# Performance work log

Hardware: AMD Instinct MI355X
Metric: run time of the kernel (lower is better)

Reference implementation:

```python
import jax, jax.numpy as jnp
import numpy as np

D = 256; NH = 8; NL = 4; NP = 4; DH = D // NH; DFFN = 1024; NQ = 900; BS = 4
SPATIAL = ((92, 92), (46, 46), (23, 23), (12, 12))  # (H, W) per level
LEVEL_START = (0, 8464, 10580, 11109)
S = sum(h * w for h, w in SPATIAL)  # 11253


def _ln(x, g, b):
    m = jnp.mean(x, -1, keepdims=True)
    v = jnp.var(x, -1, keepdims=True)
    return (x - m) / jnp.sqrt(v + 1e-5) * g + b


def setup_inputs() -> dict:
    key = jax.random.key(0)
    ks = jax.random.split(key, 24)
    p = lambda k, s: 0.02 * jax.random.normal(k, s, jnp.float32)
    return {
        "tgt": jax.random.normal(ks[0], (NQ, BS, D), jnp.float32),
        "tgt_query_pos": jax.random.normal(ks[1], (NQ, BS, D), jnp.float32),
        "tgt_reference_points": jax.random.uniform(ks[2], (NQ, BS, NL, 2), jnp.float32),
        "memory": jax.random.normal(ks[3], (S, BS, D), jnp.float32),
        "memory_spatial_shapes": jnp.array(SPATIAL, jnp.int32),
        "memory_level_start_index": jnp.array(LEVEL_START, jnp.int32),
        "in_proj_w": p(ks[4], (3 * D, D)), "in_proj_b": p(ks[5], (3 * D,)),
        "out_proj_w": p(ks[6], (D, D)), "out_proj_b": p(ks[7], (D,)),
        "off_w": p(ks[8], (NH * NL * NP * 2, D)), "off_b": p(ks[9], (NH * NL * NP * 2,)),
        "aw_w": p(ks[10], (NH * NL * NP, D)), "aw_b": p(ks[11], (NH * NL * NP,)),
        "vproj_w": p(ks[12], (D, D)), "vproj_b": p(ks[13], (D,)),
        "oproj_w": p(ks[14], (D, D)), "oproj_b": p(ks[15], (D,)),
        "ln1_g": jnp.ones((D,), jnp.float32), "ln1_b": jnp.zeros((D,), jnp.float32),
        "ln2_g": jnp.ones((D,), jnp.float32), "ln2_b": jnp.zeros((D,), jnp.float32),
        "ln3_g": jnp.ones((D,), jnp.float32), "ln3_b": jnp.zeros((D,), jnp.float32),
        "lin1_w": p(ks[16], (DFFN, D)), "lin1_b": p(ks[17], (DFFN,)),
        "lin2_w": p(ks[18], (D, DFFN)), "lin2_b": p(ks[19], (D,)),
    }


def _self_attn(q, k, v, in_w, in_b, out_w, out_b):
    # q, k, v: (nq, bs, d) -- torch nn.MultiheadAttention, eval mode
    wq, wk, wv = jnp.split(in_w, 3, axis=0)
    bq, bk, bv = jnp.split(in_b, 3)
    qp = (q @ wq.T + bq).reshape(NQ, BS, NH, DH)
    kp = (k @ wk.T + bk).reshape(NQ, BS, NH, DH)
    vp = (v @ wv.T + bv).reshape(NQ, BS, NH, DH)
    s = jnp.einsum("qbhd,kbhd->bhqk", qp, kp) / jnp.sqrt(jnp.float32(DH))
    a = jax.nn.softmax(s, axis=-1)
    o = jnp.einsum("bhqk,kbhd->qbhd", a, vp).reshape(NQ, BS, D)
    return o @ out_w.T + out_b


def _msdeform(x, ref, mem, off_w, off_b, aw_w, aw_b, vproj_w, vproj_b, oproj_w, oproj_b):
    # x: (bs, nq, d); ref: (bs, nq, nl, 2) in [0,1]; mem: (bs, S, d)
    value = (mem @ vproj_w.T + vproj_b).reshape(BS, S, NH, DH)
    off = (x @ off_w.T + off_b).reshape(BS, NQ, NH, NL, NP, 2)
    aw = jax.nn.softmax((x @ aw_w.T + aw_b).reshape(BS, NQ, NH, NL * NP), axis=-1)
    aw = aw.reshape(BS, NQ, NH, NL, NP)
    # offset normalizer = (W, H) per level
    norm = jnp.array([[w, h] for (h, w) in SPATIAL], jnp.float32)
    loc = ref[:, :, None, :, None, :] + off / norm[None, None, None, :, None, :]
    out = jnp.zeros((BS, NH, NQ, DH), x.dtype)
    for l, (H, W) in enumerate(SPATIAL):
        s0 = LEVEL_START[l]
        v = value[:, s0:s0 + H * W].transpose(0, 2, 1, 3)  # (bs, nh, H*W, dh)
        g = loc[:, :, :, l].transpose(0, 2, 1, 3, 4)       # (bs, nh, nq, np, 2)
        # grid_sample align_corners=False, padding_mode='zeros'
        px = g[..., 0] * W - 0.5
        py = g[..., 1] * H - 0.5
        x0 = jnp.floor(px).astype(jnp.int32)
        y0 = jnp.floor(py).astype(jnp.int32)
        wx = px - x0
        wy = py - y0
        samp = jnp.zeros((BS, NH, NQ, NP, DH), x.dtype)
        for dx, dy, w in ((0, 0, (1 - wx) * (1 - wy)), (1, 0, wx * (1 - wy)),
                          (0, 1, (1 - wx) * wy), (1, 1, wx * wy)):
            xi = x0 + dx
            yi = y0 + dy
            valid = ((xi >= 0) & (xi < W) & (yi >= 0) & (yi < H)).astype(x.dtype)
            idx = (jnp.clip(yi, 0, H - 1) * W + jnp.clip(xi, 0, W - 1)).reshape(BS, NH, NQ * NP)
            gat = jnp.take_along_axis(v, idx[..., None], axis=2).reshape(BS, NH, NQ, NP, DH)
            samp = samp + (w * valid)[..., None] * gat
        a = aw[:, :, :, l].transpose(0, 2, 1, 3)  # (bs, nh, nq, np)
        out = out + (samp * a[..., None]).sum(axis=3)
    out = out.transpose(0, 2, 1, 3).reshape(BS, NQ, D)
    return out @ oproj_w.T + oproj_b


def reference(tgt, tgt_query_pos, tgt_reference_points, memory,
              memory_spatial_shapes, memory_level_start_index,
              in_proj_w, in_proj_b, out_proj_w, out_proj_b,
              off_w, off_b, aw_w, aw_b, vproj_w, vproj_b, oproj_w, oproj_b,
              ln1_g, ln1_b, ln2_g, ln2_b, ln3_g, ln3_b,
              lin1_w, lin1_b, lin2_w, lin2_b):
    # module_seq = ['sa', 'ca', 'ffn']; dropout inactive (eval)
    q = tgt + tgt_query_pos
    tgt2 = _self_attn(q, q, tgt, in_proj_w, in_proj_b, out_proj_w, out_proj_b)
    tgt = _ln(tgt + tgt2, ln2_g, ln2_b)
    x = (tgt + tgt_query_pos).transpose(1, 0, 2)
    ref = tgt_reference_points.transpose(1, 0, 2, 3)
    mem = memory.transpose(1, 0, 2)
    tgt2 = _msdeform(x, ref, mem, off_w, off_b, aw_w, aw_b,
                     vproj_w, vproj_b, oproj_w, oproj_b).transpose(1, 0, 2)
    tgt = _ln(tgt + tgt2, ln1_g, ln1_b)
    ff = jax.nn.relu(tgt @ lin1_w.T + lin1_b) @ lin2_w.T + lin2_b
    return _ln(tgt + ff, ln3_g, ln3_b)
```

## Files before the change

### kernel.cpp

```cpp
#include <hip/hip_runtime.h>
#include <math.h>

#define D_MODEL 256
#define NHEAD   8
#define NLVL    4
#define NPTS    4
#define DHEAD   32
#define DFFN    1024
#define NQ      900
#define BSZ     4
#define NROW    (NQ * BSZ)
#define NROWP   3648
#define S_TOT   11253
#define VROWS   (S_TOT * BSZ)
#define SASCALE 0.17677669529663687f

typedef __attribute__((ext_vector_type(8))) short short8;
typedef __attribute__((ext_vector_type(4))) float f32x4;
typedef unsigned short ushort_t;

static __device__ __forceinline__ unsigned f2bf1(float f) {
    unsigned u = __float_as_uint(f);
    return (u + 0x7FFFu + ((u >> 16) & 1u)) >> 16;
}
static __device__ __forceinline__ unsigned pack2bf(float x, float y) {
    return f2bf1(x) | (f2bf1(y) << 16);
}
static __device__ __forceinline__ float bf2f(ushort_t u) {
    return __uint_as_float(((unsigned)u) << 16);
}

#if __has_builtin(__builtin_amdgcn_global_load_lds)
#define HAS_GLL 1
#endif

static __device__ __forceinline__ void stage_w16(const ushort_t* g, ushort_t* ldsbase, int lane)
{
#ifdef HAS_GLL
    __builtin_amdgcn_global_load_lds(
        (const __attribute__((address_space(1))) unsigned int*)g,
        (__attribute__((address_space(3))) unsigned int*)ldsbase, 16, 0, 0);
#else
    *(uint4*)(ldsbase + lane * 8) = *(const uint4*)g;
#endif
}

#define WAIT_VM_BAR(N) do {                                            \
    asm volatile("s_waitcnt vmcnt(" #N ") lgkmcnt(0)" ::: "memory");   \
    __builtin_amdgcn_sched_barrier(0);                                 \
    __builtin_amdgcn_s_barrier(); } while (0)

#define LK_BAR() do {                                                  \
    asm volatile("s_waitcnt lgkmcnt(0)" ::: "memory");                 \
    __builtin_amdgcn_sched_barrier(0);                                 \
    __builtin_amdgcn_s_barrier(); } while (0)

#define WB_IN   0
#define WB_VP   196608
#define WB_OUTP 262144
#define WB_OFF  327680
#define WB_AW   393216
#define WB_OP   425984
#define WB_L1   491520
#define WB_L2   753664
#define WB_TOT  1015808

__global__ __launch_bounds__(256) void cvt_weights(
    const float* __restrict__ w_in, const float* __restrict__ w_vp,
    const float* __restrict__ w_outp, const float* __restrict__ w_off,
    const float* __restrict__ w_aw, const float* __restrict__ w_op,
    const float* __restrict__ w_l1, const float* __restrict__ w_l2,
    ushort_t* __restrict__ dst,
    const float* __restrict__ tgt, const float* __restrict__ qpos,
    ushort_t* __restrict__ tgt16, ushort_t* __restrict__ tq16)
{
    int b = blockIdx.x;
    if (b < 496) {
        const float* src;
        int dstoff;
        int kbits = 8;
        if (b < 96)       { src = w_in;   dstoff = WB_IN;   }
        else if (b < 128) { src = w_vp;   b -= 96;  dstoff = WB_VP;   }
        else if (b < 160) { src = w_outp; b -= 128; dstoff = WB_OUTP; }
        else if (b < 192) { src = w_off;  b -= 160; dstoff = WB_OFF;  }
        else if (b < 208) { src = w_aw;   b -= 192; dstoff = WB_AW;   }
        else if (b < 240) { src = w_op;   b -= 208; dstoff = WB_OP;   }
        else if (b < 368) { src = w_l1;   b -= 240; dstoff = WB_L1;   }
        else              { src = w_l2;   b -= 368; dstoff = WB_L2;   kbits = 10; }
        int i = (b * 256 + threadIdx.x) * 8;
        float4 f0 = *(const float4*)(src + i);
        float4 f1 = *(const float4*)(src + i + 4);
        uint4 u;
        u.x = pack2bf(f0.x, f0.y); u.y = pack2bf(f0.z, f0.w);
        u.z = pack2bf(f1.x, f1.y); u.w = pack2bf(f1.z, f1.w);
        int K = 1 << kbits;
        int n = i >> kbits;
        int k = i & (K - 1);
        int kswz = (k & ~63) | ((k & 63) ^ ((n & 7) << 3));
        *(uint4*)(dst + dstoff + (size_t)n * K + kswz) = u;
    } else {
        int bb = b - 496;
        ushort_t* dbuf = tgt16;
        bool addq = false;
        if (bb >= 456) { bb -= 456; dbuf = tq16; addq = true; }
        int i = bb * 2048 + threadIdx.x * 8;
        int row = i >> 8, k = i & 255;
        uint4 u = make_uint4(0u, 0u, 0u, 0u);
        if (row < NROW) {
            const float* sp = tgt + (size_t)row * 256 + k;
            float4 f0 = *(const float4*)(sp + 0);
            float4 f1 = *(const float4*)(sp + 4);
            if (addq) {
                const float* qp = qpos + (size_t)row * 256 + k;
                float4 q0 = *(const float4*)(qp + 0);
                float4 q1 = *(const float4*)(qp + 4);
                f0.x += q0.x; f0.y += q0.y; f0.z += q0.z; f0.w += q0.w;
                f1.x += q1.x; f1.y += q1.y; f1.z += q1.z; f1.w += q1.w;
            }
            u.x = pack2bf(f0.x, f0.y); u.y = pack2bf(f0.z, f0.w);
            u.z = pack2bf(f1.x, f1.y); u.w = pack2bf(f1.z, f1.w);
        }
        int kswz = (k & ~63) | ((k & 63) ^ ((row & 7) << 3));
        *(uint4*)(dbuf + (size_t)row * 256 + kswz) = u;
    }
}

__global__ __launch_bounds__(256) void proj_fused(
    const ushort_t* __restrict__ tq16, const ushort_t* __restrict__ tgt16,
    const ushort_t* __restrict__ in_wb, const float* __restrict__ in_b,
    const float* __restrict__ mem, const ushort_t* __restrict__ vp_wb,
    const float* __restrict__ vp_b,
    ushort_t* __restrict__ qkv16, ushort_t* __restrict__ value16)
{
    __shared__ ushort_t As[2][64 * 64];
    __shared__ ushort_t Ws[2][256 * 64];

    const int t    = threadIdx.x;
    const int bid  = blockIdx.x;
    const int wv   = t >> 6;
    const int ln   = t & 63;
    const int L    = ln & 15;
    const int quad = ln >> 4;
    const int swz  = (L & 7) << 3;
    const int lrow = ln >> 3;
    const int lchk = (ln & 7) << 3;

    if (bid < 684) {
        const int m0 = (bid % 57) * 64;
        const int n0 = (bid / 57) * 64;
        const float oscale = (n0 < 256) ? SASCALE : 1.f;
        const ushort_t* Ab = (n0 < 512) ? tq16 : tgt16;

        auto stageQ = [&](int k0, int buf) {
#pragma unroll
            for (int j = 0; j < 2; ++j) {
                int r0 = (wv * 2 + j) * 8;
                stage_w16(Ab + (size_t)(m0 + r0 + lrow) * 256 + k0 + lchk, &As[buf][r0 * 64], ln);
                stage_w16(in_wb + (size_t)(n0 + r0 + lrow) * 256 + k0 + lchk, &Ws[buf][r0 * 64], ln);
            }
        };

        f32x4 acc[4] = {{0.f,0.f,0.f,0.f},{0.f,0.f,0.f,0.f},
                        {0.f,0.f,0.f,0.f},{0.f,0.f,0.f,0.f}};

        stageQ(0, 0);
        int cur = 0;
        for (int k = 0; k < 4; ++k) {
            if (k < 3) { stageQ((k + 1) * 64, cur ^ 1); WAIT_VM_BAR(4); }
            else       { WAIT_VM_BAR(0); }
#pragma unroll
            for (int kh = 0; kh < 2; ++kh) {
                int ko = (kh * 32 + quad * 8) ^ swz;
                short8 af = *(const short8*)&As[cur][(wv * 16 + L) * 64 + ko];
#pragma unroll
                for (int cb = 0; cb < 4; ++cb) {
                    short8 bf = *(const short8*)&Ws[cur][(cb * 16 + L) * 64 + ko];
                    acc[cb] = __builtin_amdgcn_mfma_f32_16x16x32_bf16(af, bf, acc[cb], 0, 0, 0);
                }
            }
            __builtin_amdgcn_s_barrier();
            cur ^= 1;
        }
#pragma unroll
        for (int cb = 0; cb < 4; ++cb) {
            int col = n0 + cb * 16 + L;
            float bv = in_b[col];
#pragma unroll
            for (int i = 0; i < 4; ++i) {
                int m = m0 + wv * 16 + quad * 4 + i;
                if (m < NROW)
                    qkv16[(size_t)m * 768 + col] = (ushort_t)f2bf1((acc[cb][i] + bv) * oscale);
            }
        }
    } else {
        const int vb = bid - 684;
        const int m0 = vb * 64;
        const int trow = t >> 2;
        const int tk   = (t & 3) << 4;
        const int wsz  = (trow & 7) << 3;

        const int  mrow = m0 + trow;
        const bool mv   = (mrow < VROWS);
        const float* arow = mem + (size_t)mrow * 256 + tk;

        auto stageWv = [&](int k0, int buf) {
#pragma unroll
            for (int j = 0; j < 8; ++j) {
                int r0 = (wv * 8 + j) * 8;
                stage_w16(vp_wb + (size_t)(r0 + lrow) * 256 + k0 + lchk, &Ws[buf][r0 * 64], ln);
            }
        };
        auto stageAv = [&](int k0, int buf) {
            uint4 u0, u1;
            if (mv) {
                const float* ap = arow + k0;
                float4 a0 = *(const float4*)(ap + 0);
                float4 a1 = *(const float4*)(ap + 4);
                float4 a2 = *(const float4*)(ap + 8);
                float4 a3 = *(const float4*)(ap + 12);
                u0.x = pack2bf(a0.x, a0.y); u0.y = pack2bf(a0.z, a0.w);
                u0.z = pack2bf(a1.x, a1.y); u0.w = pack2bf(a1.z, a1.w);
                u1.x = pack2bf(a2.x, a2.y); u1.y = pack2bf(a2.z, a2.w);
                u1.z = pack2bf(a3.x, a3.y); u1.w = pack2bf(a3.z, a3.w);
            } else {
                u0 = make_uint4(0u, 0u, 0u, 0u); u1 = u0;
            }
            *(uint4*)&As[buf][trow * 64 + (tk ^ wsz)]       = u0;
            *(uint4*)&As[buf][trow * 64 + ((tk + 8) ^ wsz)] = u1;
        };

        f32x4 acc[16];
#pragma unroll
        for (int i = 0; i < 16; ++i) acc[i] = (f32x4){0.f, 0.f, 0.f, 0.f};

        stageWv(0, 0);
        stageAv(0, 0);
        int cur = 0;
        for (int k = 0; k < 4; ++k) {
            if (k < 3) { stageWv((k + 1) * 64, cur ^ 1); WAIT_VM_BAR(8); }
            else       { WAIT_VM_BAR(0); }
#pragma unroll
            for (int kh = 0; kh < 2; ++kh) {
                int ko = (kh * 32 + quad * 8) ^ swz;
                short8 af = *(const short8*)&As[cur][(wv * 16 + L) * 64 + ko];
#pragma unroll
                for (int cb = 0; cb < 16; ++cb) {
                    short8 bf = *(const short8*)&Ws[cur][(cb * 16 + L) * 64 + ko];
                    acc[cb] = __builtin_amdgcn_mfma_f32_16x16x32_bf16(af, bf, acc[cb], 0, 0, 0);
                }
            }
            if (k < 3) stageAv((k + 1) * 64, cur ^ 1);
            __builtin_amdgcn_s_barrier();
            cur ^= 1;
        }

        ushort_t* Cs = Ws[0];
#pragma unroll
        for (int half = 0; half < 2; ++half) {
            if (half) __syncthreads();
#pragma unroll
            for (int cb = 0; cb < 8; ++cb) {
                int col = cb * 16 + L;
                float bv = vp_b[half * 128 + col];
#pragma unroll
                for (int i = 0; i < 4; ++i) {
                    int r = wv * 16 + quad * 4 + i;
                    Cs[r * 136 + col] = (ushort_t)f2bf1(acc[half * 8 + cb][i] + bv);
                }
            }
            __syncthreads();
            {
                int r  = t >> 2;
                int ch = (t & 3) * 32;
                int m  = m0 + r;
                if (m < VROWS) {
                    const ushort_t* src = &Cs[r * 136 + ch];
                    uint4* dst = (uint4*)(value16 + (size_t)m * 256 + half * 128 + ch);
#pragma unroll
                    for (int j = 0; j < 4; ++j)
                        dst[j] = *(const uint4*)(src + j * 8);
                }
            }
        }
    }
}

__global__ __launch_bounds__(256) void sa_flash16(
    const ushort_t* __restrict__ qkv, ushort_t* __restrict__ attn_out)
{
    __shared__ ushort_t Ks[2 * 2080];
    __shared__ ushort_t Vt[2 * 2304];
    __shared__ ushort_t Ps[4 * 1152];

    const int t    = threadIdx.x;
    const int q0   = blockIdx.x * 64;
    const int b    = blockIdx.y & 3;
    const int h    = blockIdx.y >> 2;
    const int wv   = t >> 6;
    const int ln   = t & 63;
    const int L    = ln & 15;
    const int quad = ln >> 4;

    union { uint4 u; short8 s; } qu;
    qu.u = make_uint4(0u, 0u, 0u, 0u);
    {
        int q = q0 + wv * 16 + L;
        if (q < NQ)
            qu.u = *(const uint4*)(qkv + ((size_t)q * 4 + b) * 768 + h * 32 + quad * 8);
    }
    const short8 qf = qu.s;

    float mrun = -1e30f, lrun = 0.f;
    f32x4 oacc[2] = {{0.f,0.f,0.f,0.f},{0.f,0.f,0.f,0.f}};

    const int skey = t >> 2;
    const int sdg  = t & 3;

    uint4 ku, vu;
    auto kv_load = [&](int k0) {
        int kg = k0 + skey;
        ku = make_uint4(0u, 0u, 0u, 0u);
        vu = make_uint4(0u, 0u, 0u, 0u);
        if (kg < NQ) {
            const ushort_t* base = qkv + ((size_t)kg * 4 + b) * 768 + 256 + h * 32 + sdg * 8;
            ku = *(const uint4*)base;
            vu = *(const uint4*)(base + 256);
        }
    };

    kv_load(0);
    int it = 0;
    for (int k0 = 0; k0 < NQ; k0 += 64, it ^= 1) {
        *(uint4*)&Ks[it * 2080 + sdg * 520 + skey * 8] = ku;
        {
            ushort_t* vp = &Vt[it * 2304 + sdg * 8 * 72 + skey];
            vp[0 * 72] = (ushort_t)(vu.x & 0xffffu);
            vp[1 * 72] = (ushort_t)(vu.x >> 16);
            vp[2 * 72] = (ushort_t)(vu.y & 0xffffu);
            vp[3 * 72] = (ushort_t)(vu.y >> 16);
            vp[4 * 72] = (ushort_t)(vu.z & 0xffffu);
            vp[5 * 72] = (ushort_t)(vu.z >> 16);
            vp[6 * 72] = (ushort_t)(vu.w & 0xffffu);
            vp[7 * 72] = (ushort_t)(vu.w >> 16);
        }
        __syncthreads();
        if (k0 + 64 < NQ) kv_load(k0 + 64);

        f32x4 sacc[4] = {{0.f,0.f,0.f,0.f},{0.f,0.f,0.f,0.f},
                         {0.f,0.f,0.f,0.f},{0.f,0.f,0.f,0.f}};
#pragma unroll
        for (int cb = 0; cb < 4; ++cb) {
            short8 kf = *(const short8*)&Ks[it * 2080 + quad * 520 + (cb * 16 + L) * 8];
            sacc[cb] = __builtin_amdgcn_mfma_f32_16x16x32_bf16(kf, qf, sacc[cb], 0, 0, 0);
        }
        if (k0 + 64 > NQ) {
#pragma unroll
            for (int cb = 0; cb < 4; ++cb)
#pragma unroll
                for (int i = 0; i < 4; ++i)
                    if (k0 + cb * 16 + quad * 4 + i >= NQ) sacc[cb][i] = -1e30f;
        }

        float ml = -1e30f;
#pragma unroll
        for (int cb = 0; cb < 4; ++cb)
#pragma unroll
            for (int i = 0; i < 4; ++i) ml = fmaxf(ml, sacc[cb][i]);
        ml = fmaxf(ml, __shfl_xor(ml, 16, 64));
        ml = fmaxf(ml, __shfl_xor(ml, 32, 64));
        float mnew  = fmaxf(mrun, ml);
        float alpha = __expf(mrun - mnew);
        float p[16];
        float rs = 0.f;
#pragma unroll
        for (int cb = 0; cb < 4; ++cb)
#pragma unroll
            for (int i = 0; i < 4; ++i) {
                float e = __expf(sacc[cb][i] - mnew);
                p[cb * 4 + i] = e;
                rs += e;
            }
        rs += __shfl_xor(rs, 16, 64);
        rs += __shfl_xor(rs, 32, 64);
        lrun = lrun * alpha + rs;
        mrun = mnew;

        {
            ushort_t* pw = &Ps[wv * 1152 + L * 72];
#pragma unroll
            for (int cb = 0; cb < 4; ++cb) {
                uint2 u;
                u.x = pack2bf(p[cb * 4 + 0], p[cb * 4 + 1]);
                u.y = pack2bf(p[cb * 4 + 2], p[cb * 4 + 3]);
                *(uint2*)&pw[cb * 16 + quad * 4] = u;
            }
        }
#pragma unroll
        for (int i = 0; i < 4; ++i) {
            float ai = __shfl(alpha, quad * 4 + i, 64);
            oacc[0][i] *= ai;
            oacc[1][i] *= ai;
        }
        __syncthreads();

#pragma unroll
        for (int ks = 0; ks < 2; ++ks) {
            short8 pf = *(const short8*)&Ps[wv * 1152 + L * 72 + ks * 32 + quad * 8];
#pragma unroll
            for (int db = 0; db < 2; ++db) {
                short8 vf = *(const short8*)&Vt[it * 2304 + (db * 16 + L) * 72 + ks * 32 + quad * 8];
                oacc[db] = __builtin_amdgcn_mfma_f32_16x16x32_bf16(pf, vf, oacc[db], 0, 0, 0);
            }
        }
    }

#pragma unroll
    for (int i = 0; i < 4; ++i) {
        float lq = __shfl(lrun, quad * 4 + i, 64);
        float li = 1.f / lq;
        int q = q0 + wv * 16 + quad * 4 + i;
        if (q < NQ) {
            ushort_t* op = attn_out + ((size_t)q * 4 + b) * 256 + h * 32 + L;
            op[0]  = (ushort_t)f2bf1(oacc[0][i] * li);
            op[16] = (ushort_t)f2bf1(oacc[1][i] * li);
        }
    }
}

__global__ __launch_bounds__(512, 1) void fused_ca(
    const ushort_t* __restrict__ att16,
    const float* __restrict__ tgt, const float* __restrict__ qpos,
    const ushort_t* __restrict__ outp_wb, const float* __restrict__ outp_b,
    const float* __restrict__ ln2g, const float* __restrict__ ln2b,
    const ushort_t* __restrict__ off_wb, const float* __restrict__ off_b,
    const ushort_t* __restrict__ aw_wb, const float* __restrict__ aw_b,
    const float* __restrict__ refp,
    float* __restrict__ tgt_a, float* __restrict__ px_g,
    float* __restrict__ py_g, float* __restrict__ aw_g)
{
    __shared__ ushort_t Ws[2][256 * 64];
    __shared__ ushort_t att_s[16 * 264];
    __shared__ ushort_t xca_s[16 * 264];
    __shared__ float    aws_s[16 * 128];
    __shared__ float    sS[8][16], s2S[8][16];

    const int t    = threadIdx.x;
    const int m0   = blockIdx.x * 16;
    const int wv   = t >> 6;
    const int ln   = t & 63;
    const int L    = ln & 15;
    const int quad = ln >> 4;
    const int swz  = (L & 7) << 3;
    const int lrow = ln >> 3;
    const int lchk = (ln & 7) << 3;
    const int rloc = quad * 4;

    auto stage4 = [&](const ushort_t* base, int buf) {
#pragma unroll
        for (int j = 0; j < 4; ++j) {
            int r0 = (wv * 4 + j) * 8;
            stage_w16(base + (size_t)(r0 + lrow) * 256 + lchk, &Ws[buf][r0 * 64], ln);
        }
    };
    auto stage2 = [&](const ushort_t* base, int buf) {
#pragma unroll
        for (int j = 0; j < 2; ++j) {
            int r0 = (wv * 2 + j) * 8;
            stage_w16(base + (size_t)(r0 + lrow) * 256 + lchk, &Ws[buf][r0 * 64], ln);
        }
    };
    auto mfma2 = [&](const ushort_t* A, int koff, int buf, f32x4* acc) {
#pragma unroll
        for (int kh = 0; kh < 2; ++kh) {
            int ko = (kh * 32 + quad * 8) ^ swz;
            short8 af = *(const short8*)&A[L * 264 + koff + kh * 32 + quad * 8];
#pragma unroll
            for (int cb = 0; cb < 2; ++cb) {
                short8 bf = *(const short8*)&Ws[buf][(wv * 32 + cb * 16 + L) * 64 + ko];
                acc[cb] = __builtin_amdgcn_mfma_f32_16x16x32_bf16(af, bf, acc[cb], 0, 0, 0);
            }
        }
    };

    {
        int r = t >> 5, s = (t & 31) * 8;
        *(uint4*)&att_s[r * 264 + s] = *(const uint4*)(att16 + (size_t)(m0 + r) * 256 + s);
    }
    stage4(outp_wb, 0);
    int cur = 0;

    {
        f32x4 acc[2] = {{0.f,0.f,0.f,0.f},{0.f,0.f,0.f,0.f}};
        for (int k = 0; k < 4; ++k) {
            if (k < 3) stage4(outp_wb + (k + 1) * 64, cur ^ 1);
            else       stage4(off_wb, cur ^ 1);
            WAIT_VM_BAR(4);
            mfma2(att_s, k * 64, cur, acc);
            __builtin_amdgcn_s_barrier();
            cur ^= 1;
        }
        float s[4] = {0.f,0.f,0.f,0.f}, s2v[4] = {0.f,0.f,0.f,0.f};
#pragma unroll
        for (int cb = 0; cb < 2; ++cb) {
            int col = wv * 32 + cb * 16 + L;
            float bv = outp_b[col];
#pragma unroll
            for (int i = 0; i < 4; ++i) {
                float xv = acc[cb][i] + bv + tgt[(size_t)(m0 + rloc + i) * 256 + col];
                acc[cb][i] = xv;
                s[i] += xv; s2v[i] += xv * xv;
            }
        }
#pragma unroll
        for (int off = 1; off < 16; off <<= 1)
#pragma unroll
            for (int i = 0; i < 4; ++i) {
                s[i]   += __shfl_xor(s[i],   off, 64);
                s2v[i] += __shfl_xor(s2v[i], off, 64);
            }
        if (L == 0)
#pragma unroll
            for (int i = 0; i < 4; ++i) { sS[wv][rloc + i] = s[i]; s2S[wv][rloc + i] = s2v[i]; }
        LK_BAR();
        float mean[4], rstd[4];
#pragma unroll
        for (int i = 0; i < 4; ++i) {
            float St = 0.f, S2t = 0.f;
#pragma unroll
            for (int w = 0; w < 8; ++w) { St += sS[w][rloc + i]; S2t += s2S[w][rloc + i]; }
            mean[i] = St * (1.f / 256.f);
            float var = S2t * (1.f / 256.f) - mean[i] * mean[i];
            rstd[i] = rsqrtf(var + 1e-5f);
        }
#pragma unroll
        for (int cb = 0; cb < 2; ++cb) {
            int col = wv * 32 + cb * 16 + L;
            float gv = ln2g[col], bt = ln2b[col];
#pragma unroll
            for (int i = 0; i < 4; ++i) {
                float y = (acc[cb][i] - mean[i]) * rstd[i] * gv + bt;
                tgt_a[(size_t)(m0 + rloc + i) * 256 + col] = y;
                xca_s[(rloc + i) * 264 + col] =
                    (ushort_t)f2bf1(y + qpos[(size_t)(m0 + rloc + i) * 256 + col]);
            }
        }
    }

    {
        f32x4 acc[2] = {{0.f,0.f,0.f,0.f},{0.f,0.f,0.f,0.f}};
        for (int k = 0; k < 4; ++k) {
            if (k < 3) { stage4(off_wb + (k + 1) * 64, cur ^ 1); WAIT_VM_BAR(4); }
            else       { stage2(aw_wb, cur ^ 1);                 WAIT_VM_BAR(2); }
            mfma2(xca_s, k * 64, cur, acc);
            __builtin_amdgcn_s_barrier();
            cur ^= 1;
        }
        const float dims[4] = {92.f, 46.f, 23.f, 12.f};
#pragma unroll
        for (int cb = 0; cb < 2; ++cb) {
            int col = wv * 32 + cb * 16 + L;
            float bv = off_b[col];
            int hh = col >> 5, lp = (col & 31) >> 1, isY = col & 1;
            int l = lp >> 2;
            float dim = dims[l];
            float* dst = isY ? py_g : px_g;
#pragma unroll
            for (int i = 0; i < 4; ++i) {
                int row = m0 + rloc + i;
                float ref = refp[((size_t)row * 4 + l) * 2 + isY];
                dst[(size_t)row * 128 + hh * 16 + lp] = ref * dim + (acc[cb][i] + bv) - 0.5f;
            }
        }
    }

    {
        f32x4 acc = {0.f, 0.f, 0.f, 0.f};
        for (int k = 0; k < 4; ++k) {
            if (k < 3) { stage2(aw_wb + (k + 1) * 64, cur ^ 1); WAIT_VM_BAR(2); }
            else       { WAIT_VM_BAR(0); }
#pragma unroll
            for (int kh = 0; kh < 2; ++kh) {
                int ko = (kh * 32 + quad * 8) ^ swz;
                short8 af = *(const short8*)&xca_s[L * 264 + k * 64 + kh * 32 + quad * 8];
                short8 bf = *(const short8*)&Ws[cur][(wv * 16 + L) * 64 + ko];
                acc = __builtin_amdgcn_mfma_f32_16x16x32_bf16(af, bf, acc, 0, 0, 0);
            }
            __builtin_amdgcn_s_barrier();
            cur ^= 1;
        }
        {
            int col = wv * 16 + L;
            float bv = aw_b[col];
#pragma unroll
            for (int i = 0; i < 4; ++i)
                aws_s[(rloc + i) * 128 + col] = acc[i] + bv;
        }
        LK_BAR();
    }

    if (t < 128) {
        int r = t >> 3, hh = t & 7;
        float v[16];
        float m = -1e30f;
#pragma unroll
        for (int j = 0; j < 16; ++j) { v[j] = aws_s[r * 128 + hh * 16 + j]; m = fmaxf(m, v[j]); }
        float ssum = 0.f;
#pragma unroll
        for (int j = 0; j < 16; ++j) { v[j] = __expf(v[j] - m); ssum += v[j]; }
        float inv = 1.f / ssum;
#pragma unroll
        for (int j = 0; j < 16; ++j)
            aw_g[(size_t)(m0 + r) * 128 + hh * 16 + j] = v[j] * inv;
    }
}

__global__ __launch_bounds__(256) void msdeform4(
    const float* __restrict__ px_g, const float* __restrict__ py_g,
    const float* __restrict__ aw_g, const ushort_t* __restrict__ value16,
    ushort_t* __restrict__ out)
{
    const int t   = threadIdx.x;
    const int row = blockIdx.x * 4 + (t >> 6);
    const int ln  = t & 63;
    const int h   = ln >> 3;
    const int d   = (ln & 7) * 4;
    const int b   = row & 3;

    const int HsI[4] = {92, 46, 23, 12};
    const int S0_[4] = {0, 8464, 10580, 11109};

    const ushort_t* vb = value16 + (size_t)b * 256 + h * 32 + d;
    const float* pxr = px_g + (size_t)row * 128 + h * 16;
    const float* pyr = py_g + (size_t)row * 128 + h * 16;
    const float* awr = aw_g + (size_t)row * 128 + h * 16;

    float a0 = 0.f, a1 = 0.f, a2 = 0.f, a3 = 0.f;
#pragma unroll
    for (int l = 0; l < 4; ++l) {
        const int H = HsI[l], W = HsI[l], base = S0_[l];
#pragma unroll
        for (int p = 0; p < 4; ++p) {
            const int lp = l * 4 + p;
            float px = pxr[lp], py = pyr[lp], aw = awr[lp];
            float x0f = floorf(px), y0f = floorf(py);
            int x0 = (int)x0f, y0 = (int)y0f;
            float wx = px - x0f, wy = py - y0f;
            float s0 = 0.f, s1 = 0.f, s2 = 0.f, s3 = 0.f;
#pragma unroll
            for (int dy = 0; dy < 2; ++dy) {
#pragma unroll
                for (int dx = 0; dx < 2; ++dx) {
                    int xi = x0 + dx, yi = y0 + dy;
                    float flag = (xi >= 0 && xi < W && yi >= 0 && yi < H) ? 1.f : 0.f;
                    int xc = xi < 0 ? 0 : (xi >= W ? W - 1 : xi);
                    int yc = yi < 0 ? 0 : (yi >= H ? H - 1 : yi);
                    float wgt = (dx ? wx : 1.f - wx) * (dy ? wy : 1.f - wy) * flag;
                    uint2 gv = *(const uint2*)(vb + (size_t)(base + yc * W + xc) * 1024);
                    s0 = fmaf(wgt, bf2f((ushort_t)(gv.x & 0xffffu)), s0);
                    s1 = fmaf(wgt, bf2f((ushort_t)(gv.x >> 16)), s1);
                    s2 = fmaf(wgt, bf2f((ushort_t)(gv.y & 0xffffu)), s2);
                    s3 = fmaf(wgt, bf2f((ushort_t)(gv.y >> 16)), s3);
                }
            }
            a0 = fmaf(aw, s0, a0);
            a1 = fmaf(aw, s1, a1);
            a2 = fmaf(aw, s2, a2);
            a3 = fmaf(aw, s3, a3);
        }
    }
    uint2 u;
    u.x = pack2bf(a0, a1);
    u.y = pack2bf(a2, a3);
    *(uint2*)(out + (size_t)row * 256 + h * 32 + d) = u;
}

__global__ __launch_bounds__(512, 1) void ffn_fused(
    const ushort_t* __restrict__ att2_16,
    const float* __restrict__ tgt_a,
    const ushort_t* __restrict__ op_wb, const float* __restrict__ op_b,
    const float* __restrict__ ln1g, const float* __restrict__ ln1b,
    const ushort_t* __restrict__ l1_wb, const float* __restrict__ l1b,
    const ushort_t* __restrict__ l2_wb, const float* __restrict__ l2b,
    const float* __restrict__ ln3g, const float* __restrict__ ln3b,
    float* __restrict__ out)
{
    __shared__ ushort_t Ws[2][256 * 64];
    __shared__ ushort_t A1[16 * 264];
    __shared__ ushort_t hc[16 * 264];
    __shared__ float    sS[8][16], s2S[8][16];

    const int t    = threadIdx.x;
    const int m0   = blockIdx.x * 16;
    const int wv   = t >> 6;
    const int ln   = t & 63;
    const int L    = ln & 15;
    const int quad = ln >> 4;
    const int swz  = (L & 7) << 3;
    const int lrow = ln >> 3;
    const int lchk = (ln & 7) << 3;
    const int rloc = quad * 4;

    auto stageWs = [&](const ushort_t* base, int stride, int buf) {
#pragma unroll
        for (int j = 0; j < 4; ++j) {
            int r0 = (wv * 4 + j) * 8;
            stage_w16(base + (size_t)(r0 + lrow) * stride + lchk, &Ws[buf][r0 * 64], ln);
        }
    };
    auto mfma2 = [&](const ushort_t* A, int koff, int buf, f32x4* acc) {
#pragma unroll
        for (int kh = 0; kh < 2; ++kh) {
            int ko = (kh * 32 + quad * 8) ^ swz;
            short8 af = *(const short8*)&A[L * 264 + koff + kh * 32 + quad * 8];
#pragma unroll
            for (int cb = 0; cb < 2; ++cb) {
                short8 bf = *(const short8*)&Ws[buf][(wv * 32 + cb * 16 + L) * 64 + ko];
                acc[cb] = __builtin_amdgcn_mfma_f32_16x16x32_bf16(af, bf, acc[cb], 0, 0, 0);
            }
        }
    };

    {
        int r = t >> 5, s = (t & 31) * 8;
        *(uint4*)&hc[r * 264 + s] = *(const uint4*)(att2_16 + (size_t)(m0 + r) * 256 + s);
    }
    stageWs(op_wb, 256, 0);
    int cur = 0;

    f32x4 resid[2];

    {
        f32x4 acc[2] = {{0.f,0.f,0.f,0.f},{0.f,0.f,0.f,0.f}};
        for (int k = 0; k < 4; ++k) {
            if (k < 3) stageWs(op_wb + (k + 1) * 64, 256, cur ^ 1);
            else       stageWs(l1_wb, 256, cur ^ 1);
            WAIT_VM_BAR(4);
            mfma2(hc, k * 64, cur, acc);
            __builtin_amdgcn_s_barrier();
            cur ^= 1;
        }
        float s[4] = {0.f,0.f,0.f,0.f}, s2v[4] = {0.f,0.f,0.f,0.f};
#pragma unroll
        for (int cb = 0; cb < 2; ++cb) {
            int col = wv * 32 + cb * 16 + L;
            float bv = op_b[col];
#pragma unroll
            for (int i = 0; i < 4; ++i) {
                float xv = acc[cb][i] + bv + tgt_a[(size_t)(m0 + rloc + i) * 256 + col];
                acc[cb][i] = xv;
                s[i] += xv; s2v[i] += xv * xv;
            }
        }
#pragma unroll
        for (int off = 1; off < 16; off <<= 1)
#pragma unroll
            for (int i = 0; i < 4; ++i) {
                s[i]   += __shfl_xor(s[i],   off, 64);
                s2v[i] += __shfl_xor(s2v[i], off, 64);
            }
        if (L == 0)
#pragma unroll
            for (int i = 0; i < 4; ++i) { sS[wv][rloc + i] = s[i]; s2S[wv][rloc + i] = s2v[i]; }
        LK_BAR();
        float mean[4], rstd[4];
#pragma unroll
        for (int i = 0; i < 4; ++i) {
            float St = 0.f, S2t = 0.f;
#pragma unroll
            for (int w = 0; w < 8; ++w) { St += sS[w][rloc + i]; S2t += s2S[w][rloc + i]; }
            mean[i] = St * (1.f / 256.f);
            float var = S2t * (1.f / 256.f) - mean[i] * mean[i];
            rstd[i] = rsqrtf(var + 1e-5f);
        }
#pragma unroll
        for (int cb = 0; cb < 2; ++cb) {
            int col = wv * 32 + cb * 16 + L;
            float gv = ln1g[col], bt = ln1b[col];
#pragma unroll
            for (int i = 0; i < 4; ++i) {
                float y = (acc[cb][i] - mean[i]) * rstd[i] * gv + bt;
                resid[cb][i] = y;
                A1[(rloc + i) * 264 + col] = (ushort_t)f2bf1(y);
            }
        }
    }

    f32x4 accf[2] = {{0.f,0.f,0.f,0.f},{0.f,0.f,0.f,0.f}};
    for (int c = 0; c < 4; ++c) {
        f32x4 acch[2] = {{0.f,0.f,0.f,0.f},{0.f,0.f,0.f,0.f}};
        for (int k = 0; k < 4; ++k) {
            if (k < 3) stageWs(l1_wb + (size_t)(c * 256) * 256 + (k + 1) * 64, 256, cur ^ 1);
            else       stageWs(l2_wb + c * 256, 1024, cur ^ 1);
            WAIT_VM_BAR(4);
            mfma2(A1, k * 64, cur, acch);
            __builtin_amdgcn_s_barrier();
            cur ^= 1;
        }
#pragma unroll
        for (int cb = 0; cb < 2; ++cb) {
            int colc = wv * 32 + cb * 16 + L;
            float bv = l1b[c * 256 + colc];
#pragma unroll
            for (int i = 0; i < 4; ++i)
                hc[(rloc + i) * 264 + colc] = (ushort_t)f2bf1(fmaxf(acch[cb][i] + bv, 0.f));
        }
        LK_BAR();
        for (int k = 0; k < 4; ++k) {
            if (k < 3)      { stageWs(l2_wb + c * 256 + (k + 1) * 64, 1024, cur ^ 1); WAIT_VM_BAR(4); }
            else if (c < 3) { stageWs(l1_wb + (size_t)((c + 1) * 256) * 256, 256, cur ^ 1); WAIT_VM_BAR(4); }
            else            { WAIT_VM_BAR(0); }
            mfma2(hc, k * 64, cur, accf);
            __builtin_amdgcn_s_barrier();
            cur ^= 1;
        }
    }

    {
        float s[4] = {0.f,0.f,0.f,0.f}, s2v[4] = {0.f,0.f,0.f,0.f};
#pragma unroll
        for (int cb = 0; cb < 2; ++cb) {
            int col = wv * 32 + cb * 16 + L;
            float bv = l2b[col];
#pragma unroll
            for (int i = 0; i < 4; ++i) {
                float xv = accf[cb][i] + bv + resid[cb][i];
                accf[cb][i] = xv;
                s[i] += xv; s2v[i] += xv * xv;
            }
        }
#pragma unroll
        for (int off = 1; off < 16; off <<= 1)
#pragma unroll
            for (int i = 0; i < 4; ++i) {
                s[i]   += __shfl_xor(s[i],   off, 64);
                s2v[i] += __shfl_xor(s2v[i], off, 64);
            }
        if (L == 0)
#pragma unroll
            for (int i = 0; i < 4; ++i) { sS[wv][rloc + i] = s[i]; s2S[wv][rloc + i] = s2v[i]; }
        LK_BAR();
        float mean[4], rstd[4];
#pragma unroll
        for (int i = 0; i < 4; ++i) {
            float St = 0.f, S2t = 0.f;
#pragma unroll
            for (int w = 0; w < 8; ++w) { St += sS[w][rloc + i]; S2t += s2S[w][rloc + i]; }
            mean[i] = St * (1.f / 256.f);
            float var = S2t * (1.f / 256.f) - mean[i] * mean[i];
            rstd[i] = rsqrtf(var + 1e-5f);
        }
#pragma unroll
        for (int cb = 0; cb < 2; ++cb) {
            int col = wv * 32 + cb * 16 + L;
            float gv = ln3g[col], bt = ln3b[col];
#pragma unroll
            for (int i = 0; i < 4; ++i) {
                float y = (accf[cb][i] - mean[i]) * rstd[i] * gv + bt;
                out[(size_t)(m0 + rloc + i) * 256 + col] = y;
            }
        }
    }
}

extern "C" void kernel_launch(void* const* d_in, const int* in_sizes, int n_in,
                              void* d_out, int out_size, void* d_ws, size_t ws_size,
                              hipStream_t stream)
{
    const float* tgt    = (const float*)d_in[0];
    const float* qpos   = (const float*)d_in[1];
    const float* refp   = (const float*)d_in[2];
    const float* mem    = (const float*)d_in[3];
    const float* in_w   = (const float*)d_in[6];
    const float* in_b   = (const float*)d_in[7];
    const float* outp_w = (const float*)d_in[8];
    const float* outp_b = (const float*)d_in[9];
    const float* off_w  = (const float*)d_in[10];
    const float* off_b  = (const float*)d_in[11];
    const float* aw_w   = (const float*)d_in[12];
    const float* aw_b   = (const float*)d_in[13];
    const float* vp_w   = (const float*)d_in[14];
    const float* vp_b   = (const float*)d_in[15];
    const float* op_w   = (const float*)d_in[16];
    const float* op_b   = (const float*)d_in[17];
    const float* ln1g   = (const float*)d_in[18];
    const float* ln1b   = (const float*)d_in[19];
    const float* ln2g   = (const float*)d_in[20];
    const float* ln2b   = (const float*)d_in[21];
    const float* ln3g   = (const float*)d_in[22];
    const float* ln3b   = (const float*)d_in[23];
    const float* l1w    = (const float*)d_in[24];
    const float* l1b    = (const float*)d_in[25];
    const float* l2w    = (const float*)d_in[26];
    const float* l2b    = (const float*)d_in[27];
    float* out = (float*)d_out;
    float* ws  = (float*)d_ws;

    ushort_t* qkv16    = (ushort_t*)ws;
    ushort_t* att16    = (ushort_t*)(ws + 691200);
    float*    tgt_a    = ws + 1843200;
    ushort_t* tgt16    = (ushort_t*)(ws + 1843200);
    ushort_t* tq16     = (ushort_t*)(ws + 2310144);
    float*    px_g     = ws + 2995200;
    float*    py_g     = ws + 3456000;
    float*    aw_g     = ws + 3916800;
    ushort_t* att2_16  = (ushort_t*)(ws + 4377600);
    ushort_t* value16  = (ushort_t*)(ws + 5760000);
    ushort_t* wb       = (ushort_t*)(ws + 13364736);

    const ushort_t* in_wb   = wb + WB_IN;
    const ushort_t* vp_wb   = wb + WB_VP;
    const ushort_t* outp_wb = wb + WB_OUTP;
    const ushort_t* off_wb  = wb + WB_OFF;
    const ushort_t* aw_wb   = wb + WB_AW;
    const ushort_t* op_wb   = wb + WB_OP;
    const ushort_t* l1_wb   = wb + WB_L1;
    const ushort_t* l2_wb   = wb + WB_L2;

    dim3 b256(256);

    hipLaunchKernelGGL(cvt_weights, dim3(1408), b256, 0, stream,
                       in_w, vp_w, outp_w, off_w, aw_w, op_w, l1w, l2w, wb,
                       tgt, qpos, tgt16, tq16);
    hipLaunchKernelGGL(proj_fused, dim3(1388), b256, 0, stream,
                       tq16, tgt16, in_wb, in_b, mem, vp_wb, vp_b, qkv16, value16);
    hipLaunchKernelGGL(sa_flash16, dim3(15, 32), b256, 0, stream, qkv16, att16);
    hipLaunchKernelGGL(fused_ca, dim3(225), dim3(512), 0, stream,
                       att16, tgt, qpos, outp_wb, outp_b, ln2g, ln2b,
                       off_wb, off_b, aw_wb, aw_b, refp,
                       tgt_a, px_g, py_g, aw_g);
    hipLaunchKernelGGL(msdeform4, dim3(900), b256, 0, stream,
                       px_g, py_g, aw_g, value16, att2_16);
    hipLaunchKernelGGL(ffn_fused, dim3(225), dim3(512), 0, stream,
                       att2_16, tgt_a, op_wb, op_b, ln1g, ln1b,
                       l1_wb, l1b, l2_wb, l2b, ln3g, ln3b, out);
}
```

Measured before the change: 242.9 us.

## Split projection kernel, halve weight LDS tiles, add MFMA priority hints

Splits the fused QKV/value projection kernel into two separate kernels so the QKV blocks no longer reserve the large 256-row weight LDS buffer. The fused_ca and ffn_fused kernels stage weights in 128-row halves instead of 256-row tiles, which halves their weight LDS footprint but doubles the number of staging/barrier steps. s_setprio hints are added around the MFMA sections in the flash attention kernel. The aim is higher occupancy from a smaller LDS footprint, at the cost of an extra launch and more synchronization rounds.

```diff
diff --git a/kernel.cpp b/kernel.cpp
--- a/kernel.cpp
+++ b/kernel.cpp
@@ -125,18 +125,15 @@
     }
 }
 
-__global__ __launch_bounds__(256) void proj_fused(
+__global__ __launch_bounds__(256) void proj_qkv(
     const ushort_t* __restrict__ tq16, const ushort_t* __restrict__ tgt16,
     const ushort_t* __restrict__ in_wb, const float* __restrict__ in_b,
-    const float* __restrict__ mem, const ushort_t* __restrict__ vp_wb,
-    const float* __restrict__ vp_b,
-    ushort_t* __restrict__ qkv16, ushort_t* __restrict__ value16)
+    ushort_t* __restrict__ qkv16)
 {
     __shared__ ushort_t As[2][64 * 64];
-    __shared__ ushort_t Ws[2][256 * 64];
+    __shared__ ushort_t Ws[2][64 * 64];
 
     const int t    = threadIdx.x;
-    const int bid  = blockIdx.x;
     const int wv   = t >> 6;
     const int ln   = t & 63;
     const int L    = ln & 15;
@@ -145,141 +142,155 @@
     const int lrow = ln >> 3;
     const int lchk = (ln & 7) << 3;
 
-    if (bid < 684) {
-        const int m0 = (bid % 57) * 64;
-        const int n0 = (bid / 57) * 64;
-        const float oscale = (n0 < 256) ? SASCALE : 1.f;
-        const ushort_t* Ab = (n0 < 512) ? tq16 : tgt16;
-
-        auto stageQ = [&](int k0, int buf) {
-#pragma unroll
-            for (int j = 0; j < 2; ++j) {
-                int r0 = (wv * 2 + j) * 8;
-                stage_w16(Ab + (size_t)(m0 + r0 + lrow) * 256 + k0 + lchk, &As[buf][r0 * 64], ln);
-                stage_w16(in_wb + (size_t)(n0 + r0 + lrow) * 256 + k0 + lchk, &Ws[buf][r0 * 64], ln);
-            }
-        };
-
-        f32x4 acc[4] = {{0.f,0.f,0.f,0.f},{0.f,0.f,0.f,0.f},
-                        {0.f,0.f,0.f,0.f},{0.f,0.f,0.f,0.f}};
-
-        stageQ(0, 0);
-        int cur = 0;
-        for (int k = 0; k < 4; ++k) {
-            if (k < 3) { stageQ((k + 1) * 64, cur ^ 1); WAIT_VM_BAR(4); }
-            else       { WAIT_VM_BAR(0); }
-#pragma unroll
-            for (int kh = 0; kh < 2; ++kh) {
-                int ko = (kh * 32 + quad * 8) ^ swz;
-                short8 af = *(const short8*)&As[cur][(wv * 16 + L) * 64 + ko];
-#pragma unroll
-                for (int cb = 0; cb < 4; ++cb) {
-                    short8 bf = *(const short8*)&Ws[cur][(cb * 16 + L) * 64 + ko];
-                    acc[cb] = __builtin_amdgcn_mfma_f32_16x16x32_bf16(af, bf, acc[cb], 0, 0, 0);
-                }
-            }
-            __builtin_amdgcn_s_barrier();
-            cur ^= 1;
-        }
-#pragma unroll
-        for (int cb = 0; cb < 4; ++cb) {
-            int col = n0 + cb * 16 + L;
-            float bv = in_b[col];
-#pragma unroll
-            for (int i = 0; i < 4; ++i) {
-                int m = m0 + wv * 16 + quad * 4 + i;
-                if (m < NROW)
-                    qkv16[(size_t)m * 768 + col] = (ushort_t)f2bf1((acc[cb][i] + bv) * oscale);
-            }
-        }
-    } else {
-        const int vb = bid - 684;
-        const int m0 = vb * 64;
-        const int trow = t >> 2;
-        const int tk   = (t & 3) << 4;
-        const int wsz  = (trow & 7) << 3;
-
-        const int  mrow = m0 + trow;
-        const bool mv   = (mrow < VROWS);
-        const float* arow = mem + (size_t)mrow * 256 + tk;
-
-        auto stageWv = [&](int k0, int buf) {
-#pragma unroll
-            for (int j = 0; j < 8; ++j) {
-                int r0 = (wv * 8 + j) * 8;
-                stage_w16(vp_wb + (size_t)(r0 + lrow) * 256 + k0 + lchk, &Ws[buf][r0 * 64], ln);
-            }
-        };
-        auto stageAv = [&](int k0, int buf) {
-            uint4 u0, u1;
-            if (mv) {
-                const float* ap = arow + k0;
-                float4 a0 = *(const float4*)(ap + 0);
-                float4 a1 = *(const float4*)(ap + 4);
-                float4 a2 = *(const float4*)(ap + 8);
-                float4 a3 = *(const float4*)(ap + 12);
-                u0.x = pack2bf(a0.x, a0.y); u0.y = pack2bf(a0.z, a0.w);
-                u0.z = pack2bf(a1.x, a1.y); u0.w = pack2bf(a1.z, a1.w);
-                u1.x = pack2bf(a2.x, a2.y); u1.y = pack2bf(a2.z, a2.w);
-                u1.z = pack2bf(a3.x, a3.y); u1.w = pack2bf(a3.z, a3.w);
-            } else {
-                u0 = make_uint4(0u, 0u, 0u, 0u); u1 = u0;
-            }
-            *(uint4*)&As[buf][trow * 64 + (tk ^ wsz)]       = u0;
-            *(uint4*)&As[buf][trow * 64 + ((tk + 8) ^ wsz)] = u1;
-        };
-
-        f32x4 acc[16];
-#pragma unroll
-        for (int i = 0; i < 16; ++i) acc[i] = (f32x4){0.f, 0.f, 0.f, 0.f};
-
-        stageWv(0, 0);
-        stageAv(0, 0);
-        int cur = 0;
-        for (int k = 0; k < 4; ++k) {
-            if (k < 3) { stageWv((k + 1) * 64, cur ^ 1); WAIT_VM_BAR(8); }
-            else       { WAIT_VM_BAR(0); }
-#pragma unroll
-            for (int kh = 0; kh < 2; ++kh) {
-                int ko = (kh * 32 + quad * 8) ^ swz;
-                short8 af = *(const short8*)&As[cur][(wv * 16 + L) * 64 + ko];
-#pragma unroll
-                for (int cb = 0; cb < 16; ++cb) {
-                    short8 bf = *(const short8*)&Ws[cur][(cb * 16 + L) * 64 + ko];
-                    acc[cb] = __builtin_amdgcn_mfma_f32_16x16x32_bf16(af, bf, acc[cb], 0, 0, 0);
-                }
-            }
-            if (k < 3) stageAv((k + 1) * 64, cur ^ 1);
-            __builtin_amdgcn_s_barrier();
-            cur ^= 1;
-        }
-
-        ushort_t* Cs = Ws[0];
-#pragma unroll
-        for (int half = 0; half < 2; ++half) {
-            if (half) __syncthreads();
-#pragma unroll
-            for (int cb = 0; cb < 8; ++cb) {
-                int col = cb * 16 + L;
-                float bv = vp_b[half * 128 + col];
-#pragma unroll
-                for (int i = 0; i < 4; ++i) {
-                    int r = wv * 16 + quad * 4 + i;
-                    Cs[r * 136 + col] = (ushort_t)f2bf1(acc[half * 8 + cb][i] + bv);
-                }
-            }
-            __syncthreads();
-            {
-                int r  = t >> 2;
-                int ch = (t & 3) * 32;
-                int m  = m0 + r;
-                if (m < VROWS) {
-                    const ushort_t* src = &Cs[r * 136 + ch];
-                    uint4* dst = (uint4*)(value16 + (size_t)m * 256 + half * 128 + ch);
-#pragma unroll
-                    for (int j = 0; j < 4; ++j)
-                        dst[j] = *(const uint4*)(src + j * 8);
-                }
+    const int m0 = (blockIdx.x % 57) * 64;
+    const int n0 = (blockIdx.x / 57) * 64;
+    const float oscale = (n0 < 256) ? SASCALE : 1.f;
+    const ushort_t* Ab = (n0 < 512) ? tq16 : tgt16;
+
+    auto stageQ = [&](int k0, int buf) {
+#pragma unroll
+        for (int j = 0; j < 2; ++j) {
+            int r0 = (wv * 2 + j) * 8;
+            stage_w16(Ab + (size_t)(m0 + r0 + lrow) * 256 + k0 + lchk, &As[buf][r0 * 64], ln);
+            stage_w16(in_wb + (size_t)(n0 + r0 + lrow) * 256 + k0 + lchk, &Ws[buf][r0 * 64], ln);
+        }
+    };
+
+    f32x4 acc[4] = {{0.f,0.f,0.f,0.f},{0.f,0.f,0.f,0.f},
+                    {0.f,0.f,0.f,0.f},{0.f,0.f,0.f,0.f}};
+
+    stageQ(0, 0);
+    int cur = 0;
+    for (int k = 0; k < 4; ++k) {
+        if (k < 3) { stageQ((k + 1) * 64, cur ^ 1); WAIT_VM_BAR(4); }
+        else       { WAIT_VM_BAR(0); }
+#pragma unroll
+        for (int kh = 0; kh < 2; ++kh) {
+            int ko = (kh * 32 + quad * 8) ^ swz;
+            short8 af = *(const short8*)&As[cur][(wv * 16 + L) * 64 + ko];
+#pragma unroll
+            for (int cb = 0; cb < 4; ++cb) {
+                short8 bf = *(const short8*)&Ws[cur][(cb * 16 + L) * 64 + ko];
+                acc[cb] = __builtin_amdgcn_mfma_f32_16x16x32_bf16(af, bf, acc[cb], 0, 0, 0);
+            }
+        }
+        __builtin_amdgcn_s_barrier();
+        cur ^= 1;
+    }
+#pragma unroll
+    for (int cb = 0; cb < 4; ++cb) {
+        int col = n0 + cb * 16 + L;
+        float bv = in_b[col];
+#pragma unroll
+        for (int i = 0; i < 4; ++i) {
+            int m = m0 + wv * 16 + quad * 4 + i;
+            if (m < NROW)
+                qkv16[(size_t)m * 768 + col] = (ushort_t)f2bf1((acc[cb][i] + bv) * oscale);
+        }
+    }
+}
+
+__global__ __launch_bounds__(256) void proj_val(
+    const float* __restrict__ mem, const ushort_t* __restrict__ vp_wb,
+    const float* __restrict__ vp_b, ushort_t* __restrict__ value16)
+{
+    __shared__ ushort_t As[2][64 * 64];
+    __shared__ ushort_t Ws[2][256 * 64];
+
+    const int t    = threadIdx.x;
+    const int wv   = t >> 6;
+    const int ln   = t & 63;
+    const int L    = ln & 15;
+    const int quad = ln >> 4;
+    const int swz  = (L & 7) << 3;
+    const int lrow = ln >> 3;
+    const int lchk = (ln & 7) << 3;
+
+    const int m0 = blockIdx.x * 64;
+    const int trow = t >> 2;
+    const int tk   = (t & 3) << 4;
+    const int wsz  = (trow & 7) << 3;
+
+    const int  mrow = m0 + trow;
+    const bool mv   = (mrow < VROWS);
+    const float* arow = mem + (size_t)mrow * 256 + tk;
+
+    auto stageWv = [&](int k0, int buf) {
+#pragma unroll
+        for (int j = 0; j < 8; ++j) {
+            int r0 = (wv * 8 + j) * 8;
+            stage_w16(vp_wb + (size_t)(r0 + lrow) * 256 + k0 + lchk, &Ws[buf][r0 * 64], ln);
+        }
+    };
+    auto stageAv = [&](int k0, int buf) {
+        uint4 u0, u1;
+        if (mv) {
+            const float* ap = arow + k0;
+            float4 a0 = *(const float4*)(ap + 0);
+            float4 a1 = *(const float4*)(ap + 4);
+            float4 a2 = *(const float4*)(ap + 8);
+            float4 a3 = *(const float4*)(ap + 12);
+            u0.x = pack2bf(a0.x, a0.y); u0.y = pack2bf(a0.z, a0.w);
+            u0.z = pack2bf(a1.x, a1.y); u0.w = pack2bf(a1.z, a1.w);
+            u1.x = pack2bf(a2.x, a2.y); u1.y = pack2bf(a2.z, a2.w);
+            u1.z = pack2bf(a3.x, a3.y); u1.w = pack2bf(a3.z, a3.w);
+        } else {
+            u0 = make_uint4(0u, 0u, 0u, 0u); u1 = u0;
+        }
+        *(uint4*)&As[buf][trow * 64 + (tk ^ wsz)]       = u0;
+        *(uint4*)&As[buf][trow * 64 + ((tk + 8) ^ wsz)] = u1;
+    };
+
+    f32x4 acc[16];
+#pragma unroll
+    for (int i = 0; i < 16; ++i) acc[i] = (f32x4){0.f, 0.f, 0.f, 0.f};
+
+    stageWv(0, 0);
+    stageAv(0, 0);
+    int cur = 0;
+    for (int k = 0; k < 4; ++k) {
+        if (k < 3) { stageWv((k + 1) * 64, cur ^ 1); WAIT_VM_BAR(8); }
+        else       { WAIT_VM_BAR(0); }
+#pragma unroll
+        for (int kh = 0; kh < 2; ++kh) {
+            int ko = (kh * 32 + quad * 8) ^ swz;
+            short8 af = *(const short8*)&As[cur][(wv * 16 + L) * 64 + ko];
+#pragma unroll
+            for (int cb = 0; cb < 16; ++cb) {
+                short8 bf = *(const short8*)&Ws[cur][(cb * 16 + L) * 64 + ko];
+                acc[cb] = __builtin_amdgcn_mfma_f32_16x16x32_bf16(af, bf, acc[cb], 0, 0, 0);
+            }
+        }
+        if (k < 3) stageAv((k + 1) * 64, cur ^ 1);
+        __builtin_amdgcn_s_barrier();
+        cur ^= 1;
+    }
+
+    ushort_t* Cs = Ws[0];
+#pragma unroll
+    for (int half = 0; half < 2; ++half) {
+        if (half) __syncthreads();
+#pragma unroll
+        for (int cb = 0; cb < 8; ++cb) {
+            int col = cb * 16 + L;
+            float bv = vp_b[half * 128 + col];
+#pragma unroll
+            for (int i = 0; i < 4; ++i) {
+                int r = wv * 16 + quad * 4 + i;
+                Cs[r * 136 + col] = (ushort_t)f2bf1(acc[half * 8 + cb][i] + bv);
+            }
+        }
+        __syncthreads();
+        {
+            int r  = t >> 2;
+            int ch = (t & 3) * 32;
+            int m  = m0 + r;
+            if (m < VROWS) {
+                const ushort_t* src = &Cs[r * 136 + ch];
+                uint4* dst = (uint4*)(value16 + (size_t)m * 256 + half * 128 + ch);
+#pragma unroll
+                for (int j = 0; j < 4; ++j)
+                    dst[j] = *(const uint4*)(src + j * 8);
             }
         }
     }
@@ -348,11 +359,13 @@
 
         f32x4 sacc[4] = {{0.f,0.f,0.f,0.f},{0.f,0.f,0.f,0.f},
                          {0.f,0.f,0.f,0.f},{0.f,0.f,0.f,0.f}};
+        __builtin_amdgcn_s_setprio(1);
 #pragma unroll
         for (int cb = 0; cb < 4; ++cb) {
             short8 kf = *(const short8*)&Ks[it * 2080 + quad * 520 + (cb * 16 + L) * 8];
             sacc[cb] = __builtin_amdgcn_mfma_f32_16x16x32_bf16(kf, qf, sacc[cb], 0, 0, 0);
         }
+        __builtin_amdgcn_s_setprio(0);
         if (k0 + 64 > NQ) {
 #pragma unroll
             for (int cb = 0; cb < 4; ++cb)
@@ -403,6 +416,7 @@
         }
         __syncthreads();
 
+        __builtin_amdgcn_s_setprio(1);
 #pragma unroll
         for (int ks = 0; ks < 2; ++ks) {
             short8 pf = *(const short8*)&Ps[wv * 1152 + L * 72 + ks * 32 + quad * 8];
@@ -412,6 +426,7 @@
                 oacc[db] = __builtin_amdgcn_mfma_f32_16x16x32_bf16(pf, vf, oacc[db], 0, 0, 0);
             }
         }
+        __builtin_amdgcn_s_setprio(0);
     }
 
 #pragma unroll
@@ -438,7 +453,7 @@
     float* __restrict__ tgt_a, float* __restrict__ px_g,
     float* __restrict__ py_g, float* __restrict__ aw_g)
 {
-    __shared__ ushort_t Ws[2][256 * 64];
+    __shared__ ushort_t Ws[2][128 * 64];
     __shared__ ushort_t att_s[16 * 264];
     __shared__ ushort_t xca_s[16 * 264];
     __shared__ float    aws_s[16 * 128];
@@ -455,30 +470,20 @@
     const int lchk = (ln & 7) << 3;
     const int rloc = quad * 4;
 
-    auto stage4 = [&](const ushort_t* base, int buf) {
-#pragma unroll
-        for (int j = 0; j < 4; ++j) {
-            int r0 = (wv * 4 + j) * 8;
-            stage_w16(base + (size_t)(r0 + lrow) * 256 + lchk, &Ws[buf][r0 * 64], ln);
-        }
-    };
-    auto stage2 = [&](const ushort_t* base, int buf) {
+    auto stage128 = [&](const ushort_t* base, int k0, int buf) {
 #pragma unroll
         for (int j = 0; j < 2; ++j) {
             int r0 = (wv * 2 + j) * 8;
-            stage_w16(base + (size_t)(r0 + lrow) * 256 + lchk, &Ws[buf][r0 * 64], ln);
+            stage_w16(base + (size_t)(r0 + lrow) * 256 + k0 + lchk, &Ws[buf][r0 * 64], ln);
         }
     };
-    auto mfma2 = [&](const ushort_t* A, int koff, int buf, f32x4* acc) {
+    auto mfma1 = [&](const ushort_t* A, int koff, int buf, f32x4* acc) {
 #pragma unroll
         for (int kh = 0; kh < 2; ++kh) {
             int ko = (kh * 32 + quad * 8) ^ swz;
             short8 af = *(const short8*)&A[L * 264 + koff + kh * 32 + quad * 8];
-#pragma unroll
-            for (int cb = 0; cb < 2; ++cb) {
-                short8 bf = *(const short8*)&Ws[buf][(wv * 32 + cb * 16 + L) * 64 + ko];
-                acc[cb] = __builtin_amdgcn_mfma_f32_16x16x32_bf16(af, bf, acc[cb], 0, 0, 0);
-            }
+            short8 bf = *(const short8*)&Ws[buf][(wv * 16 + L) * 64 + ko];
+            *acc = __builtin_amdgcn_mfma_f32_16x16x32_bf16(af, bf, *acc, 0, 0, 0);
         }
     };
 
@@ -486,28 +491,34 @@
         int r = t >> 5, s = (t & 31) * 8;
         *(uint4*)&att_s[r * 264 + s] = *(const uint4*)(att16 + (size_t)(m0 + r) * 256 + s);
     }
-    stage4(outp_wb, 0);
+    const ushort_t* outpH[2] = {outp_wb, outp_wb + 128 * 256};
+    const ushort_t* offH[2]  = {off_wb,  off_wb  + 128 * 256};
+
+    stage128(outpH[0], 0, 0);
     int cur = 0;
 
-    {
-        f32x4 acc[2] = {{0.f,0.f,0.f,0.f},{0.f,0.f,0.f,0.f}};
+    f32x4 accO[2] = {{0.f,0.f,0.f,0.f},{0.f,0.f,0.f,0.f}};
+    for (int h2 = 0; h2 < 2; ++h2) {
         for (int k = 0; k < 4; ++k) {
-            if (k < 3) stage4(outp_wb + (k + 1) * 64, cur ^ 1);
-            else       stage4(off_wb, cur ^ 1);
-            WAIT_VM_BAR(4);
-            mfma2(att_s, k * 64, cur, acc);
+            if (k < 3)       stage128(outpH[h2], (k + 1) * 64, cur ^ 1);
+            else if (h2 == 0) stage128(outpH[1], 0, cur ^ 1);
+            else              stage128(offH[0], 0, cur ^ 1);
+            WAIT_VM_BAR(2);
+            mfma1(att_s, k * 64, cur, &accO[h2]);
             __builtin_amdgcn_s_barrier();
             cur ^= 1;
         }
+    }
+    {
         float s[4] = {0.f,0.f,0.f,0.f}, s2v[4] = {0.f,0.f,0.f,0.f};
 #pragma unroll
-        for (int cb = 0; cb < 2; ++cb) {
-            int col = wv * 32 + cb * 16 + L;
+        for (int h2 = 0; h2 < 2; ++h2) {
+            int col = h2 * 128 + wv * 16 + L;
             float bv = outp_b[col];
 #pragma unroll
             for (int i = 0; i < 4; ++i) {
-                float xv = acc[cb][i] + bv + tgt[(size_t)(m0 + rloc + i) * 256 + col];
-                acc[cb][i] = xv;
+                float xv = accO[h2][i] + bv + tgt[(size_t)(m0 + rloc + i) * 256 + col];
+                accO[h2][i] = xv;
                 s[i] += xv; s2v[i] += xv * xv;
             }
         }
@@ -533,12 +544,12 @@
             rstd[i] = rsqrtf(var + 1e-5f);
         }
 #pragma unroll
-        for (int cb = 0; cb < 2; ++cb) {
-            int col = wv * 32 + cb * 16 + L;
+        for (int h2 = 0; h2 < 2; ++h2) {
+            int col = h2 * 128 + wv * 16 + L;
             float gv = ln2g[col], bt = ln2b[col];
 #pragma unroll
             for (int i = 0; i < 4; ++i) {
-                float y = (acc[cb][i] - mean[i]) * rstd[i] * gv + bt;
+                float y = (accO[h2][i] - mean[i]) * rstd[i] * gv + bt;
                 tgt_a[(size_t)(m0 + rloc + i) * 256 + col] = y;
                 xca_s[(rloc + i) * 264 + col] =
                     (ushort_t)f2bf1(y + qpos[(size_t)(m0 + rloc + i) * 256 + col]);
@@ -546,21 +557,25 @@
         }
     }
 
-    {
-        f32x4 acc[2] = {{0.f,0.f,0.f,0.f},{0.f,0.f,0.f,0.f}};
+    f32x4 accF[2] = {{0.f,0.f,0.f,0.f},{0.f,0.f,0.f,0.f}};
+    for (int h2 = 0; h2 < 2; ++h2) {
         for (int k = 0; k < 4; ++k) {
-            if (k < 3) { stage4(off_wb + (k + 1) * 64, cur ^ 1); WAIT_VM_BAR(4); }
-            else       { stage2(aw_wb, cur ^ 1);                 WAIT_VM_BAR(2); }
-            mfma2(xca_s, k * 64, cur, acc);
+            if (k < 3)        stage128(offH[h2], (k + 1) * 64, cur ^ 1);
+            else if (h2 == 0) stage128(offH[1], 0, cur ^ 1);
+            else              stage128(aw_wb, 0, cur ^ 1);
+            WAIT_VM_BAR(2);
+            mfma1(xca_s, k * 64, cur, &accF[h2]);
             __builtin_amdgcn_s_barrier();
             cur ^= 1;
         }
+    }
+    {
         const float dims[4] = {92.f, 46.f, 23.f, 12.f};
 #pragma unroll
-        for (int cb = 0; cb < 2; ++cb) {
-            int col = wv * 32 + cb * 16 + L;
+        for (int h2 = 0; h2 < 2; ++h2) {
+            int col = h2 * 128 + wv * 16 + L;
             float bv = off_b[col];
-            int hh = col >> 5, lp = (col & 31) >> 1, isY = col & 1;
+            int hd = col >> 5, lp = (col & 31) >> 1, isY = col & 1;
             int l = lp >> 2;
             float dim = dims[l];
             float* dst = isY ? py_g : px_g;
@@ -568,23 +583,17 @@
             for (int i = 0; i < 4; ++i) {
                 int row = m0 + rloc + i;
                 float ref = refp[((size_t)row * 4 + l) * 2 + isY];
-                dst[(size_t)row * 128 + hh * 16 + lp] = ref * dim + (acc[cb][i] + bv) - 0.5f;
+                dst[(size_t)row * 128 + hd * 16 + lp] = ref * dim + (accF[h2][i] + bv) - 0.5f;
             }
         }
     }
 
     {
-        f32x4 acc = {0.f, 0.f, 0.f, 0.f};
+        f32x4 accA = {0.f, 0.f, 0.f, 0.f};
         for (int k = 0; k < 4; ++k) {
-            if (k < 3) { stage2(aw_wb + (k + 1) * 64, cur ^ 1); WAIT_VM_BAR(2); }
+            if (k < 3) { stage128(aw_wb, (k + 1) * 64, cur ^ 1); WAIT_VM_BAR(2); }
             else       { WAIT_VM_BAR(0); }
-#pragma unroll
-            for (int kh = 0; kh < 2; ++kh) {
-                int ko = (kh * 32 + quad * 8) ^ swz;
-                short8 af = *(const short8*)&xca_s[L * 264 + k * 64 + kh * 32 + quad * 8];
-                short8 bf = *(const short8*)&Ws[cur][(wv * 16 + L) * 64 + ko];
-                acc = __builtin_amdgcn_mfma_f32_16x16x32_bf16(af, bf, acc, 0, 0, 0);
-            }
+            mfma1(xca_s, k * 64, cur, &accA);
             __builtin_amdgcn_s_barrier();
             cur ^= 1;
         }
@@ -593,7 +602,7 @@
             float bv = aw_b[col];
 #pragma unroll
             for (int i = 0; i < 4; ++i)
-                aws_s[(rloc + i) * 128 + col] = acc[i] + bv;
+                aws_s[(rloc + i) * 128 + col] = accA[i] + bv;
         }
         LK_BAR();
     }
@@ -684,7 +693,7 @@
     const float* __restrict__ ln3g, const float* __restrict__ ln3b,
     float* __restrict__ out)
 {
-    __shared__ ushort_t Ws[2][256 * 64];
+    __shared__ ushort_t Ws[2][128 * 64];
     __shared__ ushort_t A1[16 * 264];
     __shared__ ushort_t hc[16 * 264];
     __shared__ float    sS[8][16], s2S[8][16];
@@ -700,23 +709,20 @@
     const int lchk = (ln & 7) << 3;
     const int rloc = quad * 4;
 
-    auto stageWs = [&](const ushort_t* base, int stride, int buf) {
-#pragma unroll
-        for (int j = 0; j < 4; ++j) {
-            int r0 = (wv * 4 + j) * 8;
-            stage_w16(base + (size_t)(r0 + lrow) * stride + lchk, &Ws[buf][r0 * 64], ln);
+    auto stage128s = [&](const ushort_t* base, int stride, int k0, int buf) {
+#pragma unroll
+        for (int j = 0; j < 2; ++j) {
+            int r0 = (wv * 2 + j) * 8;
+            stage_w16(base + (size_t)(r0 + lrow) * stride + k0 + lchk, &Ws[buf][r0 * 64], ln);
         }
     };
-    auto mfma2 = [&](const ushort_t* A, int koff, int buf, f32x4* acc) {
+    auto mfma1 = [&](const ushort_t* A, int koff, int buf, f32x4* acc) {
 #pragma unroll
         for (int kh = 0; kh < 2; ++kh) {
             int ko = (kh * 32 + quad * 8) ^ swz;
             short8 af = *(const short8*)&A[L * 264 + koff + kh * 32 + quad * 8];
-#pragma unroll
-            for (int cb = 0; cb < 2; ++cb) {
-                short8 bf = *(const short8*)&Ws[buf][(wv * 32 + cb * 16 + L) * 64 + ko];
-                acc[cb] = __builtin_amdgcn_mfma_f32_16x16x32_bf16(af, bf, acc[cb], 0, 0, 0);
-            }
+            short8 bf = *(const short8*)&Ws[buf][(wv * 16 + L) * 64 + ko];
+            *acc = __builtin_amdgcn_mfma_f32_16x16x32_bf16(af, bf, *acc, 0, 0, 0);
         }
     };
 
@@ -724,30 +730,35 @@
         int r = t >> 5, s = (t & 31) * 8;
         *(uint4*)&hc[r * 264 + s] = *(const uint4*)(att2_16 + (size_t)(m0 + r) * 256 + s);
     }
-    stageWs(op_wb, 256, 0);
+    const ushort_t* opH[2] = {op_wb, op_wb + 128 * 256};
+
+    stage128s(opH[0], 256, 0, 0);
     int cur = 0;
 
     f32x4 resid[2];
 
     {
-        f32x4 acc[2] = {{0.f,0.f,0.f,0.f},{0.f,0.f,0.f,0.f}};
-        for (int k = 0; k < 4; ++k) {
-            if (k < 3) stageWs(op_wb + (k + 1) * 64, 256, cur ^ 1);
-            else       stageWs(l1_wb, 256, cur ^ 1);
-            WAIT_VM_BAR(4);
-            mfma2(hc, k * 64, cur, acc);
-            __builtin_amdgcn_s_barrier();
-            cur ^= 1;
+        f32x4 accO[2] = {{0.f,0.f,0.f,0.f},{0.f,0.f,0.f,0.f}};
+        for (int h2 = 0; h2 < 2; ++h2) {
+            for (int k = 0; k < 4; ++k) {
+                if (k < 3)        stage128s(opH[h2], 256, (k + 1) * 64, cur ^ 1);
+                else if (h2 == 0) stage128s(opH[1], 256, 0, cur ^ 1);
+                else              stage128s(l1_wb, 256, 0, cur ^ 1);
+                WAIT_VM_BAR(2);
+                mfma1(hc, k * 64, cur, &accO[h2]);
+                __builtin_amdgcn_s_barrier();
+                cur ^= 1;
+            }
         }
         float s[4] = {0.f,0.f,0.f,0.f}, s2v[4] = {0.f,0.f,0.f,0.f};
 #pragma unroll
-        for (int cb = 0; cb < 2; ++cb) {
-            int col = wv * 32 + cb * 16 + L;
+        for (int h2 = 0; h2 < 2; ++h2) {
+            int col = h2 * 128 + wv * 16 + L;
             float bv = op_b[col];
 #pragma unroll
             for (int i = 0; i < 4; ++i) {
-                float xv = acc[cb][i] + bv + tgt_a[(size_t)(m0 + rloc + i) * 256 + col];
-                acc[cb][i] = xv;
+                float xv = accO[h2][i] + bv + tgt_a[(size_t)(m0 + rloc + i) * 256 + col];
+                accO[h2][i] = xv;
                 s[i] += xv; s2v[i] += xv * xv;
             }
         }
@@ -773,13 +784,13 @@
             rstd[i] = rsqrtf(var + 1e-5f);
         }
 #pragma unroll
-        for (int cb = 0; cb < 2; ++cb) {
-            int col = wv * 32 + cb * 16 + L;
+        for (int h2 = 0; h2 < 2; ++h2) {
+            int col = h2 * 128 + wv * 16 + L;
             float gv = ln1g[col], bt = ln1b[col];
 #pragma unroll
             for (int i = 0; i < 4; ++i) {
-                float y = (acc[cb][i] - mean[i]) * rstd[i] * gv + bt;
-                resid[cb][i] = y;
+                float y = (accO[h2][i] - mean[i]) * rstd[i] * gv + bt;
+                resid[h2][i] = y;
                 A1[(rloc + i) * 264 + col] = (ushort_t)f2bf1(y);
             }
         }
@@ -787,44 +798,52 @@
 
     f32x4 accf[2] = {{0.f,0.f,0.f,0.f},{0.f,0.f,0.f,0.f}};
     for (int c = 0; c < 4; ++c) {
-        f32x4 acch[2] = {{0.f,0.f,0.f,0.f},{0.f,0.f,0.f,0.f}};
-        for (int k = 0; k < 4; ++k) {
-            if (k < 3) stageWs(l1_wb + (size_t)(c * 256) * 256 + (k + 1) * 64, 256, cur ^ 1);
-            else       stageWs(l2_wb + c * 256, 1024, cur ^ 1);
-            WAIT_VM_BAR(4);
-            mfma2(A1, k * 64, cur, acch);
-            __builtin_amdgcn_s_barrier();
-            cur ^= 1;
-        }
-#pragma unroll
-        for (int cb = 0; cb < 2; ++cb) {
-            int colc = wv * 32 + cb * 16 + L;
-            float bv = l1b[c * 256 + colc];
+        f32x4 accH[2] = {{0.f,0.f,0.f,0.f},{0.f,0.f,0.f,0.f}};
+        for (int h2 = 0; h2 < 2; ++h2) {
+            const ushort_t* l1base = l1_wb + (size_t)(c * 256 + h2 * 128) * 256;
+            for (int k = 0; k < 4; ++k) {
+                if (k < 3)        stage128s(l1base, 256, (k + 1) * 64, cur ^ 1);
+                else if (h2 == 0) stage128s(l1_wb + (size_t)(c * 256 + 128) * 256, 256, 0, cur ^ 1);
+                else              stage128s(l2_wb + c * 256, 1024, 0, cur ^ 1);
+                WAIT_VM_BAR(2);
+                mfma1(A1, k * 64, cur, &accH[h2]);
+                __builtin_amdgcn_s_barrier();
+                cur ^= 1;
+            }
+        }
+#pragma unroll
+        for (int h2 = 0; h2 < 2; ++h2) {
+            int col = h2 * 128 + wv * 16 + L;
+            float bv = l1b[c * 256 + col];
 #pragma unroll
             for (int i = 0; i < 4; ++i)
-                hc[(rloc + i) * 264 + colc] = (ushort_t)f2bf1(fmaxf(acch[cb][i] + bv, 0.f));
+                hc[(rloc + i) * 264 + col] = (ushort_t)f2bf1(fmaxf(accH[h2][i] + bv, 0.f));
         }
         LK_BAR();
-        for (int k = 0; k < 4; ++k) {
-            if (k < 3)      { stageWs(l2_wb + c * 256 + (k + 1) * 64, 1024, cur ^ 1); WAIT_VM_BAR(4); }
-            else if (c < 3) { stageWs(l1_wb + (size_t)((c + 1) * 256) * 256, 256, cur ^ 1); WAIT_VM_BAR(4); }
-            else            { WAIT_VM_BAR(0); }
-            mfma2(hc, k * 64, cur, accf);
-            __builtin_amdgcn_s_barrier();
-            cur ^= 1;
+        for (int h2 = 0; h2 < 2; ++h2) {
+            const ushort_t* l2base = l2_wb + (size_t)(h2 * 128) * 1024 + c * 256;
+            for (int k = 0; k < 4; ++k) {
+                if (k < 3)        { stage128s(l2base, 1024, (k + 1) * 64, cur ^ 1); WAIT_VM_BAR(2); }
+                else if (h2 == 0) { stage128s(l2_wb + (size_t)128 * 1024 + c * 256, 1024, 0, cur ^ 1); WAIT_VM_BAR(2); }
+                else if (c < 3)   { stage128s(l1_wb + (size_t)((c + 1) * 256) * 256, 256, 0, cur ^ 1); WAIT_VM_BAR(2); }
+                else              { WAIT_VM_BAR(0); }
+                mfma1(hc, k * 64, cur, &accf[h2]);
+                __builtin_amdgcn_s_barrier();
+                cur ^= 1;
+            }
         }
     }
 
     {
         float s[4] = {0.f,0.f,0.f,0.f}, s2v[4] = {0.f,0.f,0.f,0.f};
 #pragma unroll
-        for (int cb = 0; cb < 2; ++cb) {
-            int col = wv * 32 + cb * 16 + L;
+        for (int h2 = 0; h2 < 2; ++h2) {
+            int col = h2 * 128 + wv * 16 + L;
             float bv = l2b[col];
 #pragma unroll
             for (int i = 0; i < 4; ++i) {
-                float xv = accf[cb][i] + bv + resid[cb][i];
-                accf[cb][i] = xv;
+                float xv = accf[h2][i] + bv + resid[h2][i];
+                accf[h2][i] = xv;
                 s[i] += xv; s2v[i] += xv * xv;
             }
         }
@@ -850,12 +869,12 @@
             rstd[i] = rsqrtf(var + 1e-5f);
         }
 #pragma unroll
-        for (int cb = 0; cb < 2; ++cb) {
-            int col = wv * 32 + cb * 16 + L;
+        for (int h2 = 0; h2 < 2; ++h2) {
+            int col = h2 * 128 + wv * 16 + L;
             float gv = ln3g[col], bt = ln3b[col];
 #pragma unroll
             for (int i = 0; i < 4; ++i) {
-                float y = (accf[cb][i] - mean[i]) * rstd[i] * gv + bt;
+                float y = (accf[h2][i] - mean[i]) * rstd[i] * gv + bt;
                 out[(size_t)(m0 + rloc + i) * 256 + col] = y;
             }
         }
@@ -921,8 +940,10 @@
     hipLaunchKernelGGL(cvt_weights, dim3(1408), b256, 0, stream,
                        in_w, vp_w, outp_w, off_w, aw_w, op_w, l1w, l2w, wb,
                        tgt, qpos, tgt16, tq16);
-    hipLaunchKernelGGL(proj_fused, dim3(1388), b256, 0, stream,
-                       tq16, tgt16, in_wb, in_b, mem, vp_wb, vp_b, qkv16, value16);
+    hipLaunchKernelGGL(proj_qkv, dim3(684), b256, 0, stream,
+                       tq16, tgt16, in_wb, in_b, qkv16);
+    hipLaunchKernelGGL(proj_val, dim3(704), b256, 0, stream,
+                       mem, vp_wb, vp_b, value16);
     hipLaunchKernelGGL(sa_flash16, dim3(15, 32), b256, 0, stream, qkv16, att16);
     hipLaunchKernelGGL(fused_ca, dim3(225), dim3(512), 0, stream,
                        att16, tgt, qpos, outp_wb, outp_b, ln2g, ln2b,
```

New measurement: 246.9 us. About the same (+1.6%).
